# Performance work log

Measured on AMD Instinct MI355X. Metric: run time of the kernel, lower is better.

The kernel has to match this reference:

```python
import jax, jax.numpy as jnp
import numpy as np

N = 6144
D = 128
TAU = 0.1
ADJ_P = 0.005  # edge density


def _l2_normalize(x, eps=1e-12):
    # matches torch F.normalize: x / max(||x||, eps)
    n = jnp.sqrt(jnp.sum(x * x, axis=-1, keepdims=True))
    return x / jnp.maximum(n, eps)


def setup_inputs() -> dict:
    key = jax.random.key(0)
    ks = jax.random.split(key, 8)
    embF = jax.random.normal(ks[0], (N, D), jnp.float32)
    embM = jax.random.normal(ks[1], (N, D), jnp.float32)
    embP = jax.random.normal(ks[2], (N, D), jnp.float32)
    FM_adj = (jax.random.uniform(ks[3], (N, N)) < ADJ_P).astype(jnp.float32)
    FP_adj = (jax.random.uniform(ks[4], (N, N)) < ADJ_P).astype(jnp.float32)
    W1 = jax.random.normal(ks[5], (2 * D, D), jnp.float32) * (1.0 / np.sqrt(2 * D))
    b1 = jnp.zeros((D,), jnp.float32)
    W2 = jax.random.normal(ks[6], (D, 2), jnp.float32) * (1.0 / np.sqrt(D))
    b2 = jnp.zeros((2,), jnp.float32)
    return {"embF": embF, "embM": embM, "embP": embP,
            "FM_adj": FM_adj, "FP_adj": FP_adj,
            "W1": W1, "b1": b1, "W2": W2, "b2": b2}


def reference(embF, embM, embP, FM_adj, FP_adj, W1, b1, W2, b2):
    # attention-weighted neighbor aggregation
    FM_repr = (FM_adj @ embM) / jnp.maximum(FM_adj.sum(1, keepdims=True), 1.0)
    FP_repr = (FP_adj @ embP) / jnp.maximum(FP_adj.sum(1, keepdims=True), 1.0)
    # stack(dim=1).view(N,-1) == concat along feature dim
    feat = jnp.concatenate([FM_repr, FP_repr], axis=1)            # [N, 2D]
    h = jnp.maximum(feat @ W1 + b1, 0.0)                           # ReLU (dropout inactive in eval)
    weights = jax.nn.softmax(h @ W2 + b2, axis=-1)                 # [N, 2]

    Fn = _l2_normalize(embF)
    Mn = _l2_normalize(embM)
    Pn = _l2_normalize(embP)

    FM_sim = jnp.exp((Fn @ Mn.T) / TAU)                            # [N, Nm]
    FP_sim = jnp.exp((Fn @ Pn.T) / TAU)                            # [N, Np]

    FM_pos = jnp.sum(FM_sim * FM_adj, axis=1)
    FP_pos = jnp.sum(FP_sim * FP_adj, axis=1)
    FM_neg = jnp.sum(FM_sim, axis=1) - FM_pos
    FP_neg = jnp.sum(FP_sim, axis=1) - FP_pos

    w0, w1w = weights[:, 0], weights[:, 1]
    wp = w0 * FM_pos + w1w * FP_pos
    wn = w0 * FM_neg + w1w * FP_neg

    nei_count = jnp.maximum(FM_adj.sum(1) + FP_adj.sum(1), 1.0)
    ratio = wp / (wp + wn) / nei_count
    ratio = jnp.maximum(ratio, 1e-10)
    loss = jnp.mean(-jnp.log(ratio))
    return loss, weights
```

## Files before the change

kernel.cpp:

```cpp
#include <hip/hip_runtime.h>
#include <hip/hip_bf16.h>

#define NN 6144
#define DD 128
#define PBL 136
#define INV_TAU 10.0f

typedef __attribute__((ext_vector_type(4))) float f32x4;
typedef __attribute__((ext_vector_type(8))) short s16x8;

__device__ __forceinline__ void ld4_async(const float4* p, float4& d) {
    asm volatile("global_load_dwordx4 %0, %1, off" : "=v"(d) : "v"(p));
}
__device__ __forceinline__ void vm_wait0() {
    asm volatile("s_waitcnt vmcnt(0)" ::: "memory");
}

__global__ void k_normalize(const float* __restrict__ embF,
                            const float* __restrict__ embM,
                            const float* __restrict__ embP,
                            const float* __restrict__ W1,
                            float* __restrict__ Fn,
                            float* __restrict__ rnM, float* __restrict__ rnP,
                            __hip_bfloat16* __restrict__ Fnb,
                            __hip_bfloat16* __restrict__ Mnb,
                            __hip_bfloat16* __restrict__ Pnb,
                            __hip_bfloat16* __restrict__ W1tb) {
    int which = blockIdx.y;
    if (which == 3) {
        if (blockIdx.x < 128) {
            int n = blockIdx.x, c = threadIdx.x;
            W1tb[n * 256 + c] = __float2bfloat16(W1[c * DD + n]);
        }
        return;
    }
    const float* src = which == 0 ? embF : (which == 1 ? embM : embP);
    __hip_bfloat16* dstb = which == 0 ? Fnb : (which == 1 ? Mnb : Pnb);
    int wave = threadIdx.x >> 6, lane = threadIdx.x & 63;
    int row = blockIdx.x * 4 + wave;
    float2 v = reinterpret_cast<const float2*>(src + (size_t)row * DD)[lane];
    float s = v.x * v.x + v.y * v.y;
#pragma unroll
    for (int m = 1; m <= 32; m <<= 1) s += __shfl_xor(s, m);
    float inv = 1.0f / fmaxf(sqrtf(s), 1e-12f);
    float2 o; o.x = v.x * inv; o.y = v.y * inv;
    if (which == 0)
        reinterpret_cast<float2*>(Fn + (size_t)row * DD)[lane] = o;
    if (lane == 0) {
        if (which == 1) rnM[row] = inv;
        if (which == 2) rnP[row] = inv;
    }
    __hip_bfloat162 ob;
    ob.x = __float2bfloat16(o.x);
    ob.y = __float2bfloat16(o.y);
    reinterpret_cast<__hip_bfloat162*>(dstb + (size_t)row * DD)[lane] = ob;
}

__device__ __forceinline__ void scan_body(
        int s, char* smem,
        const float* __restrict__ FM_adj, const float* __restrict__ FP_adj,
        const float* __restrict__ embM, const float* __restrict__ embP,
        const float* __restrict__ Fn,
        const float* __restrict__ rnM, const float* __restrict__ rnP,
        __hip_bfloat16* __restrict__ featb,
        float* __restrict__ FMpos, float* __restrict__ FPpos,
        float* __restrict__ cntF, float* __restrict__ cntP) {
    const int tid = threadIdx.x, w = tid >> 6, lane = tid & 63;
    unsigned short* listS = reinterpret_cast<unsigned short*>(smem) + w * 128;
    const int unit = s * 4 + w;
    const int row = unit >> 1, h = unit & 1;
    const float* adj  = h ? FP_adj : FM_adj;
    const float* embX = h ? embP : embM;
    const float* RN   = h ? rnP : rnM;
    const unsigned long long lt = (1ull << lane) - 1ull;

    float2 f2 = reinterpret_cast<const float2*>(Fn + (size_t)row * DD)[lane];
    const float4* ar = reinterpret_cast<const float4*>(adj + (size_t)row * NN);

    int cnt = 0;
    auto scan4 = [&](const float4& v, int k) {
        unsigned long long b;
        int base = k * 256 + lane * 4;
        b = __ballot(v.x != 0.f);
        if (v.x != 0.f) { int p = cnt + (int)__popcll(b & lt); if (p < 128) listS[p] = (unsigned short)base; }
        cnt += (int)__popcll(b);
        b = __ballot(v.y != 0.f);
        if (v.y != 0.f) { int p = cnt + (int)__popcll(b & lt); if (p < 128) listS[p] = (unsigned short)(base + 1); }
        cnt += (int)__popcll(b);
        b = __ballot(v.z != 0.f);
        if (v.z != 0.f) { int p = cnt + (int)__popcll(b & lt); if (p < 128) listS[p] = (unsigned short)(base + 2); }
        cnt += (int)__popcll(b);
        b = __ballot(v.w != 0.f);
        if (v.w != 0.f) { int p = cnt + (int)__popcll(b & lt); if (p < 128) listS[p] = (unsigned short)(base + 3); }
        cnt += (int)__popcll(b);
    };

    float4 va0 = ar[0 * 64 + lane], va1 = ar[1 * 64 + lane];
    float4 va2 = ar[2 * 64 + lane], va3 = ar[3 * 64 + lane];
    for (int kb = 0; kb < 24; kb += 8) {
        float4 vb0 = ar[(kb + 4) * 64 + lane], vb1 = ar[(kb + 5) * 64 + lane];
        float4 vb2 = ar[(kb + 6) * 64 + lane], vb3 = ar[(kb + 7) * 64 + lane];
        scan4(va0, kb + 0); scan4(va1, kb + 1);
        scan4(va2, kb + 2); scan4(va3, kb + 3);
        if (kb + 8 < 24) {
            va0 = ar[(kb + 8) * 64 + lane];  va1 = ar[(kb + 9) * 64 + lane];
            va2 = ar[(kb + 10) * 64 + lane]; va3 = ar[(kb + 11) * 64 + lane];
        }
        scan4(vb0, kb + 4); scan4(vb1, kb + 5);
        scan4(vb2, kb + 6); scan4(vb3, kb + 7);
    }

    asm volatile("s_waitcnt lgkmcnt(0)" ::: "memory");
    const int K = cnt < 128 ? cnt : 128;
    const float2* ex = reinterpret_cast<const float2*>(embX);
    float2 e0 = {0.f, 0.f}, e1 = {0.f, 0.f}, e2 = {0.f, 0.f}, e3 = {0.f, 0.f};
    float rr0 = 0.f, rr1 = 0.f, rr2 = 0.f, rr3 = 0.f;
#define PREF(i, E, R) if ((i) < K) { int j = listS[(i)]; E = ex[(size_t)j * 64 + lane]; R = RN[j]; }
    PREF(0, e0, rr0) PREF(1, e1, rr1) PREF(2, e2, rr2) PREF(3, e3, rr3)
    float2 racc = {0.f, 0.f};
    float wsum = 0.f;
    for (int kk = 0; kk < K; kk += 4) {
#define STEP(i, E, R)                                                        \
        if (kk + (i) < K) {                                                  \
            float2 ev = E; float rv = R;                                     \
            PREF(kk + (i) + 4, E, R)                                         \
            float d = f2.x * ev.x + f2.y * ev.y;                             \
            d += __shfl_xor(d, 1);  d += __shfl_xor(d, 2);                   \
            d += __shfl_xor(d, 4);  d += __shfl_xor(d, 8);                   \
            d += __shfl_xor(d, 16); d += __shfl_xor(d, 32);                  \
            racc.x += ev.x; racc.y += ev.y;                                  \
            wsum += __expf(d * rv * INV_TAU);                                \
        }
        STEP(0, e0, rr0) STEP(1, e1, rr1) STEP(2, e2, rr2) STEP(3, e3, rr3)
    }
#undef STEP
#undef PREF

    float invK = 1.0f / fmaxf((float)cnt, 1.0f);
    __hip_bfloat162 ob;
    ob.x = __float2bfloat16(racc.x * invK);
    ob.y = __float2bfloat16(racc.y * invK);
    reinterpret_cast<__hip_bfloat162*>(featb + (size_t)row * 256 + h * DD)[lane] = ob;
    if (lane == 0) {
        (h ? FPpos : FMpos)[row] = wsum;
        (h ? cntP : cntF)[row] = (float)cnt;
    }
}

__device__ __forceinline__ void dense_body(
        int unit, char* smem,
        const __hip_bfloat16* __restrict__ Fnb,
        const __hip_bfloat16* __restrict__ Mnb,
        const __hip_bfloat16* __restrict__ Pnb,
        float* __restrict__ FMtot, float* __restrict__ FPtot) {
    __hip_bfloat16 (*Bs)[PBL] = (__hip_bfloat16(*)[PBL])smem;
    const int bx = unit % 48, by = (unit / 48) % 16, half = unit / 768;
    const __hip_bfloat16* Bnb = half ? Pnb : Mnb;
    float* TOT = half ? FPtot : FMtot;
    const int tid = threadIdx.x;
    const int w = tid >> 6, lane = tid & 63;
    const int m = lane & 15, q = lane >> 4;
    const int rb = bx * 128 + w * 32;
    const int j0 = by * (NN / 16);

    s16x8 a[2][4];
#pragma unroll
    for (int g = 0; g < 2; ++g)
#pragma unroll
        for (int ks = 0; ks < 4; ++ks)
            a[g][ks] = *reinterpret_cast<const s16x8*>(
                Fnb + (size_t)(rb + g * 16 + m) * DD + ks * 32 + q * 8);

    float4 s0, s1, s2, s3;
    auto issue = [&](int jc) {
        const float4* gp = reinterpret_cast<const float4*>(Bnb + (size_t)jc * DD);
        ld4_async(gp + tid,       s0);
        ld4_async(gp + 256 + tid, s1);
        ld4_async(gp + 512 + tid, s2);
        ld4_async(gp + 768 + tid, s3);
    };
    auto stash = [&](int idx, const float4& v) {
        *reinterpret_cast<float4*>(&Bs[idx >> 4][(idx & 15) * 8]) = v;
    };

    issue(j0);
    float tot[2][4] = {{0.f, 0.f, 0.f, 0.f}, {0.f, 0.f, 0.f, 0.f}};
    for (int it = 0; it < 6; ++it) {
        vm_wait0();
        __syncthreads();
        stash(tid, s0);
        stash(256 + tid, s1);
        stash(512 + tid, s2);
        stash(768 + tid, s3);
        __syncthreads();
        if (it + 1 < 6) issue(j0 + (it + 1) * 64);
#pragma unroll
        for (int t = 0; t < 4; ++t) {
            s16x8 b[4];
#pragma unroll
            for (int ks = 0; ks < 4; ++ks)
                b[ks] = *reinterpret_cast<const s16x8*>(
                    &Bs[t * 16 + m][ks * 32 + q * 8]);
#pragma unroll
            for (int g = 0; g < 2; ++g) {
                f32x4 acc = {0.f, 0.f, 0.f, 0.f};
#pragma unroll
                for (int ks = 0; ks < 4; ++ks)
                    acc = __builtin_amdgcn_mfma_f32_16x16x32_bf16(
                        a[g][ks], b[ks], acc, 0, 0, 0);
#pragma unroll
                for (int r = 0; r < 4; ++r)
                    tot[g][r] += __expf(acc[r] * INV_TAU);
            }
        }
    }
#pragma unroll
    for (int msk = 1; msk <= 8; msk <<= 1)
#pragma unroll
        for (int g = 0; g < 2; ++g)
#pragma unroll
            for (int r = 0; r < 4; ++r)
                tot[g][r] += __shfl_xor(tot[g][r], msk);
    if (m == 0)
#pragma unroll
        for (int g = 0; g < 2; ++g)
#pragma unroll
            for (int r = 0; r < 4; ++r)
                atomicAdd(&TOT[rb + g * 16 + q * 4 + r], tot[g][r]);
}

__global__ __launch_bounds__(256) void k_main(
        const float* __restrict__ FM_adj, const float* __restrict__ FP_adj,
        const float* __restrict__ embM, const float* __restrict__ embP,
        const float* __restrict__ Fn,
        const float* __restrict__ rnM, const float* __restrict__ rnP,
        const __hip_bfloat16* __restrict__ Fnb,
        const __hip_bfloat16* __restrict__ Mnb,
        const __hip_bfloat16* __restrict__ Pnb,
        __hip_bfloat16* __restrict__ featb,
        float* __restrict__ FMpos, float* __restrict__ FPpos,
        float* __restrict__ FMtot, float* __restrict__ FPtot,
        float* __restrict__ cntF, float* __restrict__ cntP) {
    __shared__ char smem[64 * PBL * 2];
    const int b = blockIdx.x;
    const int u = b / 3, r = b - u * 3;
    if (r == 2)
        dense_body(u, smem, Fnb, Mnb, Pnb, FMtot, FPtot);
    else
        scan_body(u * 2 + r, smem, FM_adj, FP_adj, embM, embP,
                  Fn, rnM, rnP, featb, FMpos, FPpos, cntF, cntP);
}

__global__ __launch_bounds__(256) void k_mlp2(
        const __hip_bfloat16* __restrict__ featb,
        const __hip_bfloat16* __restrict__ W1tb,
        const float* __restrict__ b1, const float* __restrict__ W2,
        float* __restrict__ z) {
    const int tid = threadIdx.x, w = tid >> 6, lane = tid & 63;
    const int m = lane & 15, q = lane >> 4;
    const int unit = blockIdx.x * 4 + w;
    const int rb = (unit >> 3) * 16, n0 = (unit & 7) * 16;
    f32x4 acc = {0.f, 0.f, 0.f, 0.f};
#pragma unroll
    for (int ks = 0; ks < 8; ++ks) {
        s16x8 a = *reinterpret_cast<const s16x8*>(
            featb + (size_t)(rb + m) * 256 + ks * 32 + q * 8);
        s16x8 b = *reinterpret_cast<const s16x8*>(
            W1tb + (size_t)(n0 + m) * 256 + ks * 32 + q * 8);
        acc = __builtin_amdgcn_mfma_f32_16x16x32_bf16(a, b, acc, 0, 0, 0);
    }
    const int n = n0 + m;
    float bias = b1[n], w20 = W2[2 * n], w21 = W2[2 * n + 1];
#pragma unroll
    for (int r = 0; r < 4; ++r) {
        float h = fmaxf(acc[r] + bias, 0.f);
        float p0 = h * w20, p1 = h * w21;
#pragma unroll
        for (int msk = 1; msk <= 8; msk <<= 1) {
            p0 += __shfl_xor(p0, msk);
            p1 += __shfl_xor(p1, msk);
        }
        if (m == 0) {
            int row = rb + q * 4 + r;
            atomicAdd(&z[2 * row], p0);
            atomicAdd(&z[2 * row + 1], p1);
        }
    }
}

__global__ void k_loss(const float* __restrict__ z, const float* __restrict__ b2,
                       const float* __restrict__ FMpos, const float* __restrict__ FPpos,
                       const float* __restrict__ FMtot, const float* __restrict__ FPtot,
                       const float* __restrict__ cntF, const float* __restrict__ cntP,
                       float* __restrict__ out) {
    __shared__ float red[4];
    const int tid = threadIdx.x;
    const int lane = tid & 63, wv = tid >> 6;
    const int row = blockIdx.x * 256 + tid;
    float z0 = z[row * 2] + b2[0], z1 = z[row * 2 + 1] + b2[1];
    float mx = fmaxf(z0, z1);
    float e0 = expf(z0 - mx), e1 = expf(z1 - mx);
    float inv = 1.0f / (e0 + e1);
    float w0 = e0 * inv, w1 = e1 * inv;
    out[1 + row * 2 + 0] = w0;
    out[1 + row * 2 + 1] = w1;
    float wp = w0 * FMpos[row] + w1 * FPpos[row];
    float wn = w0 * (FMtot[row] - FMpos[row]) + w1 * (FPtot[row] - FPpos[row]);
    float nei = fmaxf(cntF[row] + cntP[row], 1.0f);
    float ratio = wp / (wp + wn) / nei;
    ratio = fmaxf(ratio, 1e-10f);
    float term = -logf(ratio);
#pragma unroll
    for (int msk = 1; msk <= 32; msk <<= 1) term += __shfl_xor(term, msk);
    if (lane == 0) red[wv] = term;
    __syncthreads();
    if (tid == 0)
        atomicAdd(out, (red[0] + red[1] + red[2] + red[3]) * (1.0f / NN));
}

extern "C" void kernel_launch(void* const* d_in, const int* in_sizes, int n_in,
                              void* d_out, int out_size, void* d_ws, size_t ws_size,
                              hipStream_t stream) {
    const float* embF   = (const float*)d_in[0];
    const float* embM   = (const float*)d_in[1];
    const float* embP   = (const float*)d_in[2];
    const float* FM_adj = (const float*)d_in[3];
    const float* FP_adj = (const float*)d_in[4];
    const float* W1     = (const float*)d_in[5];
    const float* b1     = (const float*)d_in[6];
    const float* W2     = (const float*)d_in[7];
    const float* b2     = (const float*)d_in[8];
    float* out = (float*)d_out;

    float* ws = (float*)d_ws;
    float* FMtot = ws;
    float* FPtot = FMtot + NN;
    float* zbuf  = FPtot + NN;
    float* FMpos = zbuf + 2 * NN;
    float* FPpos = FMpos + NN;
    float* cntF  = FPpos + NN;
    float* cntP  = cntF + NN;
    float* rnM   = cntP + NN;
    float* rnP   = rnM + NN;
    float* Fn    = rnP + NN;
    __hip_bfloat16* Fnb = (__hip_bfloat16*)(Fn + (size_t)NN * DD);
    __hip_bfloat16* Mnb = Fnb + (size_t)NN * DD;
    __hip_bfloat16* Pnb = Mnb + (size_t)NN * DD;
    __hip_bfloat16* featb = Pnb + (size_t)NN * DD;
    __hip_bfloat16* W1tb  = featb + (size_t)NN * 256;

    hipMemsetAsync(FMtot, 0, 4 * NN * sizeof(float), stream);
    hipMemsetAsync(d_out, 0, sizeof(float), stream);

    k_normalize<<<dim3(NN / 4, 4), 256, 0, stream>>>(embF, embM, embP, W1,
                                                     Fn, rnM, rnP,
                                                     Fnb, Mnb, Pnb, W1tb);
    k_main<<<dim3(4608), 256, 0, stream>>>(FM_adj, FP_adj, embM, embP,
                                           Fn, rnM, rnP, Fnb, Mnb, Pnb,
                                           featb, FMpos, FPpos, FMtot, FPtot,
                                           cntF, cntP);
    k_mlp2<<<dim3(768), 256, 0, stream>>>(featb, W1tb, b1, W2, zbuf);
    k_loss<<<dim3(NN / 256), 256, 0, stream>>>(zbuf, b2, FMpos, FPpos,
                                               FMtot, FPtot, cntF, cntP, out);
}
```

Baseline: 379.3 us.

## Split fused scan/dense kernel into separate k_scan and k_dense launches

Replaces the single k_main kernel, which interleaved adjacency-scan blocks with dense similarity-matmul blocks, with two separate kernels launched back to back. Each kernel gets its own shared memory sizing and register allocation, which may improve occupancy for the lighter scan path. In exchange it gives up concurrent overlap of the memory-bound adjacency scan with the compute-bound exp-sum matmul, and adds a launch boundary.

```diff
diff --git a/kernel.cpp b/kernel.cpp
--- a/kernel.cpp
+++ b/kernel.cpp
@@ -56,8 +56,7 @@
     reinterpret_cast<__hip_bfloat162*>(dstb + (size_t)row * DD)[lane] = ob;
 }
 
-__device__ __forceinline__ void scan_body(
-        int s, char* smem,
+__global__ __launch_bounds__(256) void k_scan(
         const float* __restrict__ FM_adj, const float* __restrict__ FP_adj,
         const float* __restrict__ embM, const float* __restrict__ embP,
         const float* __restrict__ Fn,
@@ -65,9 +64,10 @@
         __hip_bfloat16* __restrict__ featb,
         float* __restrict__ FMpos, float* __restrict__ FPpos,
         float* __restrict__ cntF, float* __restrict__ cntP) {
+    __shared__ unsigned short listAll[4][128];
     const int tid = threadIdx.x, w = tid >> 6, lane = tid & 63;
-    unsigned short* listS = reinterpret_cast<unsigned short*>(smem) + w * 128;
-    const int unit = s * 4 + w;
+    unsigned short* listS = listAll[w];
+    const int unit = blockIdx.x * 4 + w;
     const int row = unit >> 1, h = unit & 1;
     const float* adj  = h ? FP_adj : FM_adj;
     const float* embX = h ? embP : embM;
@@ -147,13 +147,13 @@
     }
 }
 
-__device__ __forceinline__ void dense_body(
-        int unit, char* smem,
+__global__ __launch_bounds__(256) void k_dense(
         const __hip_bfloat16* __restrict__ Fnb,
         const __hip_bfloat16* __restrict__ Mnb,
         const __hip_bfloat16* __restrict__ Pnb,
         float* __restrict__ FMtot, float* __restrict__ FPtot) {
-    __hip_bfloat16 (*Bs)[PBL] = (__hip_bfloat16(*)[PBL])smem;
+    __shared__ __hip_bfloat16 Bs[64][PBL];
+    const int unit = blockIdx.x;
     const int bx = unit % 48, by = (unit / 48) % 16, half = unit / 768;
     const __hip_bfloat16* Bnb = half ? Pnb : Mnb;
     float* TOT = half ? FPtot : FMtot;
@@ -227,28 +227,6 @@
 #pragma unroll
             for (int r = 0; r < 4; ++r)
                 atomicAdd(&TOT[rb + g * 16 + q * 4 + r], tot[g][r]);
-}
-
-__global__ __launch_bounds__(256) void k_main(
-        const float* __restrict__ FM_adj, const float* __restrict__ FP_adj,
-        const float* __restrict__ embM, const float* __restrict__ embP,
-        const float* __restrict__ Fn,
-        const float* __restrict__ rnM, const float* __restrict__ rnP,
-        const __hip_bfloat16* __restrict__ Fnb,
-        const __hip_bfloat16* __restrict__ Mnb,
-        const __hip_bfloat16* __restrict__ Pnb,
-        __hip_bfloat16* __restrict__ featb,
-        float* __restrict__ FMpos, float* __restrict__ FPpos,
-        float* __restrict__ FMtot, float* __restrict__ FPtot,
-        float* __restrict__ cntF, float* __restrict__ cntP) {
-    __shared__ char smem[64 * PBL * 2];
-    const int b = blockIdx.x;
-    const int u = b / 3, r = b - u * 3;
-    if (r == 2)
-        dense_body(u, smem, Fnb, Mnb, Pnb, FMtot, FPtot);
-    else
-        scan_body(u * 2 + r, smem, FM_adj, FP_adj, embM, embP,
-                  Fn, rnM, rnP, featb, FMpos, FPpos, cntF, cntP);
 }
 
 __global__ __launch_bounds__(256) void k_mlp2(
@@ -355,10 +333,10 @@
     k_normalize<<<dim3(NN / 4, 4), 256, 0, stream>>>(embF, embM, embP, W1,
                                                      Fn, rnM, rnP,
                                                      Fnb, Mnb, Pnb, W1tb);
-    k_main<<<dim3(4608), 256, 0, stream>>>(FM_adj, FP_adj, embM, embP,
-                                           Fn, rnM, rnP, Fnb, Mnb, Pnb,
-                                           featb, FMpos, FPpos, FMtot, FPtot,
-                                           cntF, cntP);
+    k_scan<<<dim3(3072), 256, 0, stream>>>(FM_adj, FP_adj, embM, embP,
+                                           Fn, rnM, rnP,
+                                           featb, FMpos, FPpos, cntF, cntP);
+    k_dense<<<dim3(1536), 256, 0, stream>>>(Fnb, Mnb, Pnb, FMtot, FPtot);
     k_mlp2<<<dim3(768), 256, 0, stream>>>(featb, W1tb, b1, W2, zbuf);
     k_loss<<<dim3(NN / 256), 256, 0, stream>>>(zbuf, b2, FMpos, FPpos,
                                                FMtot, FPtot, cntF, cntP, out);
```

Result: slower. 399.7 us (+5.4%).
